# Performance work log

Measured on AMD Instinct MI355X. Metric: run time of the kernel, lower is better.

## Reference

```python
import jax, jax.numpy as jnp
import numpy as np

T, G, K, N = 8192, 8, 1024, 2048

def setup_inputs() -> dict:
    key = jax.random.key(0)
    k1, k2, k3 = jax.random.split(key, 3)
    x = jax.random.normal(k1, (T, K), dtype=jnp.float32)
    w = jax.random.normal(k2, (G, N, K), dtype=jnp.float32) * 0.02
    # cumulative end-offsets per group: sorted, last entry == T (covers all tokens)
    offs = jnp.sort(jax.random.randint(k3, (G,), 0, T).astype(jnp.int32))
    offs = offs.at[-1].set(T)
    return {"input": x, "weight": w, "grouped_mm_offs": offs}

def reference(input, weight, grouped_mm_offs):
    # grouped_mm(input, weight.transpose(1,2), offs): token t in group g iff
    # offs[g-1] <= t < offs[g]; out[t] = input[t] @ weight[g].T
    t = input.shape[0]
    g = weight.shape[0]
    gid = jnp.searchsorted(grouped_mm_offs, jnp.arange(t), side="right")  # [T]
    out = jnp.zeros((t, weight.shape[1]), dtype=input.dtype)
    for gi in range(g):  # fixed small expert loop; data dims stay vectorized
        xg = jnp.where((gid == gi)[:, None], input, jnp.zeros((), input.dtype))
        out = out + xg @ weight[gi].T
    return out
```

## Files before the change

### kernel.cpp

```cpp
#include <hip/hip_runtime.h>
#include <hip/hip_bf16.h>


#define T_DIM 8192
#define G_DIM 8
#define K_DIM 1024
#define N_DIM 2048
#define MAX_PAIRS 40
#define NT (K_DIM / 64)

using short8  = __attribute__((ext_vector_type(8))) short;
using f32x4   = __attribute__((ext_vector_type(4))) float;
using ushort8 = __attribute__((ext_vector_type(8))) unsigned short;

typedef __attribute__((address_space(1))) void gvoid;
typedef __attribute__((address_space(3))) void lvoid;

#define FENCE() asm volatile("" ::: "memory")

__global__ __launch_bounds__(256) void cvt_kernel(const float* __restrict__ x,
                                                  const float* __restrict__ w,
                                                  ushort8* __restrict__ xb,
                                                  ushort8* __restrict__ wb,
                                                  int n8x, int n8tot) {
  const int stride = gridDim.x * blockDim.x;
  for (int i = blockIdx.x * blockDim.x + threadIdx.x; i < n8tot; i += 2 * stride) {
#pragma unroll
    for (int u = 0; u < 2; ++u) {
      const int idx = i + u * stride;
      if (idx >= n8tot) break;
      const f32x4* s; ushort8* d; int j;
      if (idx < n8x) { s = (const f32x4*)x; d = xb; j = idx; }
      else           { s = (const f32x4*)w; d = wb; j = idx - n8x; }
      f32x4 v0 = __builtin_nontemporal_load(&s[2 * j]);
      f32x4 v1 = __builtin_nontemporal_load(&s[2 * j + 1]);
      ushort8 o;
      o[0] = __builtin_bit_cast(unsigned short, __float2bfloat16(v0[0]));
      o[1] = __builtin_bit_cast(unsigned short, __float2bfloat16(v0[1]));
      o[2] = __builtin_bit_cast(unsigned short, __float2bfloat16(v0[2]));
      o[3] = __builtin_bit_cast(unsigned short, __float2bfloat16(v0[3]));
      o[4] = __builtin_bit_cast(unsigned short, __float2bfloat16(v1[0]));
      o[5] = __builtin_bit_cast(unsigned short, __float2bfloat16(v1[1]));
      o[6] = __builtin_bit_cast(unsigned short, __float2bfloat16(v1[2]));
      o[7] = __builtin_bit_cast(unsigned short, __float2bfloat16(v1[3]));
      d[j] = o;
    }
  }
}

__global__ __launch_bounds__(512, 2) void grouped_gemm_kernel(
    const __hip_bfloat16* __restrict__ xb,
    const __hip_bfloat16* __restrict__ wb,
    const int* __restrict__ offs,
    float* __restrict__ out) {
  const int v  = blockIdx.y * 16 + blockIdx.x;
  const int c  = v & 7;
  const int l  = v >> 3;
  const int p  = c * 5 + (l % 5);
  const int nb = l / 5;
  const int n0 = nb * 128;

  int offv[G_DIM];
#pragma unroll
  for (int i = 0; i < G_DIM; ++i) offv[i] = offs[i];

  int g = -1, tile = 0, lo = 0, hi = 0, pre = 0;
#pragma unroll
  for (int gi = 0; gi < G_DIM; ++gi) {
    const int lb = gi ? offv[gi - 1] : 0;
    const int hb = offv[gi];
    const int t0 = lb >> 8;
    const int cnt = (hb > lb) ? (((hb + 255) >> 8) - t0) : 0;
    if (g < 0 && p < pre + cnt) { g = gi; tile = t0 + (p - pre); lo = lb; hi = hb; }
    pre += cnt;
  }
  if (g < 0) return;

  const int m0 = tile * 256;

  __shared__ __align__(16) __hip_bfloat16 Ar[4][128 * 64];
  __shared__ __align__(16) __hip_bfloat16 Br[4][64 * 64];

  const __hip_bfloat16* wg = wb + (size_t)g * N_DIM * K_DIM;

  const int lane = threadIdx.x & 63;
  const int wid  = threadIdx.x >> 6;
  const int wm   = wid >> 1;
  const int wn   = wid & 1;

  const int srow = lane >> 3;
  const int scol = ((lane & 7) ^ srow) * 8;

  const __hip_bfloat16* aSrc0 = xb + (size_t)(m0 + srow) * K_DIM + scol;
  const __hip_bfloat16* bSrc0 = wg + (size_t)(n0 + srow) * K_DIM + scol;

  auto stageA = [&](int tt, int hi) {
    const int slot = (2 * tt + hi) & 3;
#pragma unroll
    for (int i = 0; i < 2; ++i) {
      const int ch = wid * 2 + i;
      const __hip_bfloat16* src = aSrc0 + (size_t)(hi * 128 + ch * 8) * K_DIM + tt * 64;
      __builtin_amdgcn_global_load_lds((gvoid*)src,
                                       (lvoid*)(&Ar[slot][ch * 512 + lane * 8]),
                                       16, 0, 0);
    }
  };
  auto stageB = [&](int tt, int hi) {
    const int slot = (2 * tt + hi) & 3;
    const __hip_bfloat16* src = bSrc0 + (size_t)(hi * 64 + wid * 8) * K_DIM + tt * 64;
    __builtin_amdgcn_global_load_lds((gvoid*)src,
                                     (lvoid*)(&Br[slot][wid * 512 + lane * 8]),
                                     16, 0, 0);
  };

  f32x4 acc[4][4] = {};

  stageA(0, 0); stageA(0, 1);
  stageB(0, 0); stageB(0, 1);
  stageA(1, 0); stageA(1, 1);
  asm volatile("s_waitcnt vmcnt(4)" ::: "memory");
  __builtin_amdgcn_s_barrier();
  FENCE();

  const int ahalf = wm >> 1;
  const int arow0 = (wm & 1) * 64;

  for (int kt = 0; kt < NT; ++kt) {
    const int sA = (2 * kt + ahalf) & 3;
    const int sB = (2 * kt + wn) & 3;
    short8 a[4][2];

#pragma unroll
    for (int nf = 0; nf < 4; ++nf) {
      if (nf == 0) {
#pragma unroll
        for (int mf = 0; mf < 4; ++mf)
#pragma unroll
          for (int ks = 0; ks < 2; ++ks) {
            const int off = (((ks * 4 + (lane >> 4)) ^ (lane & 7)) * 8);
            a[mf][ks] = *reinterpret_cast<const short8*>(
                &Ar[sA][(arow0 + mf * 16 + (lane & 15)) * 64 + off]);
          }
      }
      short8 b0, b1;
      {
        const int row = nf * 16 + (lane & 15);
        const int o0  = (((0 * 4 + (lane >> 4)) ^ (lane & 7)) * 8);
        const int o1  = (((1 * 4 + (lane >> 4)) ^ (lane & 7)) * 8);
        b0 = *reinterpret_cast<const short8*>(&Br[sB][row * 64 + o0]);
        b1 = *reinterpret_cast<const short8*>(&Br[sB][row * 64 + o1]);
      }

      if (nf == 1 && kt + 1 < NT) { stageB(kt + 1, 0); stageB(kt + 1, 1); }
      if (nf == 2 && kt + 2 < NT) { stageA(kt + 2, 0); }
      if (nf == 3) {
        if (kt + 2 < NT) stageA(kt + 2, 1);
        if (kt < NT - 2) {
          asm volatile("s_waitcnt vmcnt(4)" ::: "memory");
        } else {
          asm volatile("s_waitcnt vmcnt(0)" ::: "memory");
        }
      }

      FENCE();
      __builtin_amdgcn_s_barrier();
      FENCE();

      __builtin_amdgcn_s_setprio(1);
#pragma unroll
      for (int mf = 0; mf < 4; ++mf) {
        acc[mf][nf] = __builtin_amdgcn_mfma_f32_16x16x32_bf16(
            a[mf][0], b0, acc[mf][nf], 0, 0, 0);
        acc[mf][nf] = __builtin_amdgcn_mfma_f32_16x16x32_bf16(
            a[mf][1], b1, acc[mf][nf], 0, 0, 0);
      }
      __builtin_amdgcn_s_setprio(0);

      FENCE();
      __builtin_amdgcn_s_barrier();
      FENCE();
    }
  }

  const int quad = lane >> 4;
#pragma unroll
  for (int mf = 0; mf < 4; ++mf) {
    const int rbase = m0 + wm * 64 + mf * 16 + quad * 4;
#pragma unroll
    for (int r = 0; r < 4; ++r) {
      const int row = rbase + r;
      if (row < lo || row >= hi) continue;
#pragma unroll
      for (int nf = 0; nf < 4; ++nf) {
        const int col = n0 + wn * 64 + nf * 16 + (lane & 15);
        out[(size_t)row * N_DIM + col] = acc[mf][nf][r];
      }
    }
  }
}

__global__ __launch_bounds__(256) void fallback_kernel(
    const float* __restrict__ x, const float* __restrict__ w,
    const int* __restrict__ offs, float* __restrict__ out) {
  __shared__ float xs[K_DIM];
  const int t = blockIdx.y;
  int g = 0;
  while (g < G_DIM - 1 && offs[g] <= t) ++g;
  for (int i = threadIdx.x; i < K_DIM; i += blockDim.x)
    xs[i] = x[(size_t)t * K_DIM + i];
  __syncthreads();
  const int n = blockIdx.x * blockDim.x + threadIdx.x;
  const float* wr = w + ((size_t)g * N_DIM + n) * K_DIM;
  float s = 0.f;
  for (int k = 0; k < K_DIM; ++k) s += xs[k] * wr[k];
  out[(size_t)t * N_DIM + n] = s;
}

extern "C" void kernel_launch(void* const* d_in, const int* in_sizes, int n_in,
                              void* d_out, int out_size, void* d_ws, size_t ws_size,
                              hipStream_t stream) {
  const float* x    = (const float*)d_in[0];
  const float* w    = (const float*)d_in[1];
  const int*   offs = (const int*)d_in[2];
  float*       out  = (float*)d_out;

  const size_t x_elems = (size_t)T_DIM * K_DIM;
  const size_t w_elems = (size_t)G_DIM * N_DIM * K_DIM;
  const size_t need    = (x_elems + w_elems) * sizeof(__hip_bfloat16);

  if (ws_size < need) {
    fallback_kernel<<<dim3(N_DIM / 256, T_DIM), 256, 0, stream>>>(x, w, offs, out);
    return;
  }

  __hip_bfloat16* xb = (__hip_bfloat16*)d_ws;
  __hip_bfloat16* wb = xb + x_elems;

  const int n8x   = (int)(x_elems / 8);
  const int n8tot = (int)((x_elems + w_elems) / 8);
  cvt_kernel<<<4096, 256, 0, stream>>>(x, w, (ushort8*)xb, (ushort8*)wb,
                                       n8x, n8tot);

  grouped_gemm_kernel<<<dim3(16, MAX_PAIRS), 512, 0, stream>>>(
      xb, wb, offs, out);
}
```

Baseline: 214.9 us.

## Widen GEMM block tile to 256x256 with 2x4 wave layout

Doubles the N extent of each workgroup's output tile from 128 to 256 and halves the grid. The 8 waves are rearranged into a 2x4 grid, each computing 128x64 with 8x4 accumulator fragments. B staging now loads four 64-row quarters per k-step, with adjusted LDS slots and wait counts. This raises reuse of each loaded A tile and cuts global traffic, at the cost of more LDS (about 128KB), more registers per thread, and fewer blocks, which may hurt occupancy and CU load balance.

After: 211.4 us. About the same (-1.7%).

```diff
diff --git a/kernel.cpp b/kernel.cpp
--- a/kernel.cpp
+++ b/kernel.cpp
@@ -53,12 +53,12 @@
     const __hip_bfloat16* __restrict__ wb,
     const int* __restrict__ offs,
     float* __restrict__ out) {
-  const int v  = blockIdx.y * 16 + blockIdx.x;
+  const int v  = blockIdx.y * 8 + blockIdx.x;
   const int c  = v & 7;
   const int l  = v >> 3;
   const int p  = c * 5 + (l % 5);
   const int nb = l / 5;
-  const int n0 = nb * 128;
+  const int n0 = nb * 256;
 
   int offv[G_DIM];
 #pragma unroll
@@ -78,86 +78,81 @@
 
   const int m0 = tile * 256;
 
-  __shared__ __align__(16) __hip_bfloat16 Ar[4][128 * 64];
-  __shared__ __align__(16) __hip_bfloat16 Br[4][64 * 64];
+  __shared__ __align__(16) __hip_bfloat16 Ar[4 * 128 * 64];
+  __shared__ __align__(16) __hip_bfloat16 Br[8 * 64 * 64];
 
   const __hip_bfloat16* wg = wb + (size_t)g * N_DIM * K_DIM;
 
   const int lane = threadIdx.x & 63;
   const int wid  = threadIdx.x >> 6;
-  const int wm   = wid >> 1;
-  const int wn   = wid & 1;
+  const int wm   = wid >> 2;
+  const int wn   = wid & 3;
 
   const int srow = lane >> 3;
   const int scol = ((lane & 7) ^ srow) * 8;
 
-  const __hip_bfloat16* aSrc0 = xb + (size_t)(m0 + srow) * K_DIM + scol;
-  const __hip_bfloat16* bSrc0 = wg + (size_t)(n0 + srow) * K_DIM + scol;
-
-  auto stageA = [&](int tt, int hi) {
-    const int slot = (2 * tt + hi) & 3;
+  auto stageA = [&](int tt, int h) {
+    const int slot = (tt & 1) * 2 + h;
 #pragma unroll
     for (int i = 0; i < 2; ++i) {
       const int ch = wid * 2 + i;
-      const __hip_bfloat16* src = aSrc0 + (size_t)(hi * 128 + ch * 8) * K_DIM + tt * 64;
-      __builtin_amdgcn_global_load_lds((gvoid*)src,
-                                       (lvoid*)(&Ar[slot][ch * 512 + lane * 8]),
-                                       16, 0, 0);
+      const __hip_bfloat16* src =
+          xb + (size_t)(m0 + h * 128 + ch * 8 + srow) * K_DIM + tt * 64 + scol;
+      __builtin_amdgcn_global_load_lds(
+          (gvoid*)src, (lvoid*)(Ar + slot * 8192 + ch * 512 + lane * 8), 16, 0, 0);
     }
   };
-  auto stageB = [&](int tt, int hi) {
-    const int slot = (2 * tt + hi) & 3;
-    const __hip_bfloat16* src = bSrc0 + (size_t)(hi * 64 + wid * 8) * K_DIM + tt * 64;
-    __builtin_amdgcn_global_load_lds((gvoid*)src,
-                                     (lvoid*)(&Br[slot][wid * 512 + lane * 8]),
-                                     16, 0, 0);
+  auto stageB = [&](int tt, int q) {
+    const int slot = (tt & 1) * 4 + q;
+    const __hip_bfloat16* src =
+        wg + (size_t)(n0 + q * 64 + wid * 8 + srow) * K_DIM + tt * 64 + scol;
+    __builtin_amdgcn_global_load_lds(
+        (gvoid*)src, (lvoid*)(Br + slot * 4096 + wid * 512 + lane * 8), 16, 0, 0);
   };
 
-  f32x4 acc[4][4] = {};
+  f32x4 acc[8][4] = {};
 
   stageA(0, 0); stageA(0, 1);
-  stageB(0, 0); stageB(0, 1);
+  stageB(0, 0); stageB(0, 1); stageB(0, 2); stageB(0, 3);
   stageA(1, 0); stageA(1, 1);
   asm volatile("s_waitcnt vmcnt(4)" ::: "memory");
   __builtin_amdgcn_s_barrier();
   FENCE();
 
-  const int ahalf = wm >> 1;
-  const int arow0 = (wm & 1) * 64;
-
-  for (int kt = 0; kt < NT; ++kt) {
-    const int sA = (2 * kt + ahalf) & 3;
-    const int sB = (2 * kt + wn) & 3;
-    short8 a[4][2];
-
-#pragma unroll
-    for (int nf = 0; nf < 4; ++nf) {
-      if (nf == 0) {
-#pragma unroll
-        for (int mf = 0; mf < 4; ++mf)
+  for (int t = 0; t < NT; ++t) {
+    const int abase = ((t & 1) * 2 + wm) * 8192;
+    const int bbase = ((t & 1) * 4 + wn) * 4096;
+    short8 a[8][2];
+
+#pragma unroll
+    for (int ph = 0; ph < 4; ++ph) {
+      if (ph == 0) {
+#pragma unroll
+        for (int mf = 0; mf < 8; ++mf)
 #pragma unroll
           for (int ks = 0; ks < 2; ++ks) {
             const int off = (((ks * 4 + (lane >> 4)) ^ (lane & 7)) * 8);
             a[mf][ks] = *reinterpret_cast<const short8*>(
-                &Ar[sA][(arow0 + mf * 16 + (lane & 15)) * 64 + off]);
+                Ar + abase + (mf * 16 + (lane & 15)) * 64 + off);
           }
       }
       short8 b0, b1;
       {
-        const int row = nf * 16 + (lane & 15);
-        const int o0  = (((0 * 4 + (lane >> 4)) ^ (lane & 7)) * 8);
-        const int o1  = (((1 * 4 + (lane >> 4)) ^ (lane & 7)) * 8);
-        b0 = *reinterpret_cast<const short8*>(&Br[sB][row * 64 + o0]);
-        b1 = *reinterpret_cast<const short8*>(&Br[sB][row * 64 + o1]);
-      }
-
-      if (nf == 1 && kt + 1 < NT) { stageB(kt + 1, 0); stageB(kt + 1, 1); }
-      if (nf == 2 && kt + 2 < NT) { stageA(kt + 2, 0); }
-      if (nf == 3) {
-        if (kt + 2 < NT) stageA(kt + 2, 1);
-        if (kt < NT - 2) {
+        const int row = ph * 16 + (lane & 15);
+        const int o0  = (((lane >> 4) ^ (lane & 7)) * 8);
+        const int o1  = (((4 + (lane >> 4)) ^ (lane & 7)) * 8);
+        b0 = *reinterpret_cast<const short8*>(Br + bbase + row * 64 + o0);
+        b1 = *reinterpret_cast<const short8*>(Br + bbase + row * 64 + o1);
+      }
+
+      if (ph == 0 && t + 1 < NT) { stageB(t + 1, 0); stageB(t + 1, 1); }
+      if (ph == 1 && t + 1 < NT) { stageB(t + 1, 2); stageB(t + 1, 3); }
+      if (ph == 2 && t + 2 < NT) { stageA(t + 2, 0); }
+      if (ph == 3) {
+        if (t + 2 < NT) {
+          stageA(t + 2, 1);
           asm volatile("s_waitcnt vmcnt(4)" ::: "memory");
-        } else {
+        } else if (t + 1 < NT) {
           asm volatile("s_waitcnt vmcnt(0)" ::: "memory");
         }
       }
@@ -168,11 +163,11 @@
 
       __builtin_amdgcn_s_setprio(1);
 #pragma unroll
-      for (int mf = 0; mf < 4; ++mf) {
-        acc[mf][nf] = __builtin_amdgcn_mfma_f32_16x16x32_bf16(
-            a[mf][0], b0, acc[mf][nf], 0, 0, 0);
-        acc[mf][nf] = __builtin_amdgcn_mfma_f32_16x16x32_bf16(
-            a[mf][1], b1, acc[mf][nf], 0, 0, 0);
+      for (int mf = 0; mf < 8; ++mf) {
+        acc[mf][ph] = __builtin_amdgcn_mfma_f32_16x16x32_bf16(
+            a[mf][0], b0, acc[mf][ph], 0, 0, 0);
+        acc[mf][ph] = __builtin_amdgcn_mfma_f32_16x16x32_bf16(
+            a[mf][1], b1, acc[mf][ph], 0, 0, 0);
       }
       __builtin_amdgcn_s_setprio(0);
 
@@ -184,8 +179,8 @@
 
   const int quad = lane >> 4;
 #pragma unroll
-  for (int mf = 0; mf < 4; ++mf) {
-    const int rbase = m0 + wm * 64 + mf * 16 + quad * 4;
+  for (int mf = 0; mf < 8; ++mf) {
+    const int rbase = m0 + wm * 128 + mf * 16 + quad * 4;
 #pragma unroll
     for (int r = 0; r < 4; ++r) {
       const int row = rbase + r;
@@ -241,6 +236,6 @@
   cvt_kernel<<<4096, 256, 0, stream>>>(x, w, (ushort8*)xb, (ushort8*)wb,
                                        n8x, n8tot);
 
-  grouped_gemm_kernel<<<dim3(16, MAX_PAIRS), 512, 0, stream>>>(
+  grouped_gemm_kernel<<<dim3(8, MAX_PAIRS), 512, 0, stream>>>(
       xb, wb, offs, out);
 }
```
